# Kernel tuning notes

Hardware: AMD Instinct MI355X
Metric: run time of the kernel (lower is better)

Reference implementation:

```python
import jax, jax.numpy as jnp
import numpy as np

SEQ_LEN = 8192
HIDDEN = 4096

def setup_inputs() -> dict:
    key = jax.random.key(0)
    k1, k2 = jax.random.split(key)
    hidden = jax.random.normal(k1, (HIDDEN,), dtype=jnp.float32)
    encoder_outputs = jax.random.normal(k2, (SEQ_LEN, 1, HIDDEN), dtype=jnp.float32)
    return {"hidden": hidden, "encoder_outputs": encoder_outputs}

def reference(hidden, encoder_outputs):
    # encoder_outputs: [S, 1, H] -> [S, H]
    enc = encoder_outputs.squeeze(1)
    # energies[i] = dot(hidden, enc[i])  (one batched GEMV instead of a per-step loop)
    energies = enc @ hidden  # [S]
    attn = jax.nn.softmax(energies, axis=0)  # [S]
    # output = enc^T @ attn  (torch.mm(enc.T, attn.unsqueeze(1)).squeeze(1))
    output = enc.T @ attn  # [H]
    return output, attn[:, None]
```

## Files before the change

### kernel.cpp

```cpp
#include <hip/hip_runtime.h>
#include <math.h>

#define S_LEN 8192
#define HDIM  4096
#define H4    (HDIM / 4)
#define P1_BLOCK 512
#define P1_WAVES 8
#define RB 4
#define FB_ATTN 8

__device__ __forceinline__ float wave_reduce_sum(float x) {
#pragma unroll
  for (int o = 32; o > 0; o >>= 1) x += __shfl_xor(x, o, 64);
  return x;
}
__device__ __forceinline__ float wave_reduce_max(float x) {
#pragma unroll
  for (int o = 32; o > 0; o >>= 1) x = fmaxf(x, __shfl_xor(x, o, 64));
  return x;
}
__device__ __forceinline__ float dot4(float4 a, float4 b) {
  return a.x * b.x + a.y * b.y + a.z * b.z + a.w * b.w;
}
__device__ __forceinline__ float upd(float a, float sc, const float* w,
                                     float x0, float x1, float x2, float x3) {
  float r = a * sc;
  r = fmaf(w[0], x0, r);
  r = fmaf(w[1], x1, r);
  r = fmaf(w[2], x2, r);
  r = fmaf(w[3], x3, r);
  return r;
}

__global__ __launch_bounds__(P1_BLOCK) void pass1_k(
    const float* __restrict__ enc, const float* __restrict__ hidden,
    float* __restrict__ energies, float* __restrict__ mb, float* __restrict__ lb,
    float* __restrict__ opart, int rpb) {
  const int t = threadIdx.x;
  const int b = blockIdx.x;
  const int row0 = b * rpb;
  const int row1 = min(S_LEN, row0 + rpb);

  const float4* hv = (const float4*)hidden;
  const float4 h0 = hv[t];
  const float4 h1 = hv[t + P1_BLOCK];

  float4 a0 = {0.f, 0.f, 0.f, 0.f};
  float4 a1 = {0.f, 0.f, 0.f, 0.f};
  float m = -INFINITY, l = 0.f;

  __shared__ float red[RB * P1_WAVES];
  const int wid = t >> 6;
  const bool lane0 = (t & 63) == 0;
  const float4* encv = (const float4*)enc;

  for (int r0 = row0; r0 < row1; r0 += RB) {
    const int nr = min(RB, row1 - r0);
    float4 v[RB][2];
    float d[RB];
#pragma unroll
    for (int r = 0; r < RB; ++r) {
      if (r < nr) {
        const float4* rp = encv + (size_t)(r0 + r) * H4;
        v[r][0] = rp[t];
        v[r][1] = rp[t + P1_BLOCK];
      } else {
        v[r][0] = make_float4(0.f, 0.f, 0.f, 0.f);
        v[r][1] = make_float4(0.f, 0.f, 0.f, 0.f);
      }
    }
#pragma unroll
    for (int r = 0; r < RB; ++r)
      d[r] = dot4(v[r][0], h0) + dot4(v[r][1], h1);
#pragma unroll
    for (int o = 32; o > 0; o >>= 1) {
#pragma unroll
      for (int r = 0; r < RB; ++r) d[r] += __shfl_xor(d[r], o, 64);
    }
    if (lane0) {
#pragma unroll
      for (int r = 0; r < RB; ++r) red[r * P1_WAVES + wid] = d[r];
    }
    __syncthreads();
    float e[RB];
#pragma unroll
    for (int r = 0; r < RB; ++r) {
      const float4 q0 = *(const float4*)&red[r * P1_WAVES];
      const float4 q1 = *(const float4*)&red[r * P1_WAVES + 4];
      e[r] = (q0.x + q0.y + q0.z + q0.w) + (q1.x + q1.y + q1.z + q1.w);
    }
    __syncthreads();
    if (t == 0) {
      for (int r = 0; r < nr; ++r) energies[r0 + r] = e[r];
    }
    float mn = m;
#pragma unroll
    for (int r = 0; r < RB; ++r)
      if (r < nr) mn = fmaxf(mn, e[r]);
    const float sc = __expf(m - mn);
    float w[RB];
#pragma unroll
    for (int r = 0; r < RB; ++r) w[r] = (r < nr) ? __expf(e[r] - mn) : 0.f;
    l = l * sc + w[0] + w[1] + w[2] + w[3];
    a0.x = upd(a0.x, sc, w, v[0][0].x, v[1][0].x, v[2][0].x, v[3][0].x);
    a0.y = upd(a0.y, sc, w, v[0][0].y, v[1][0].y, v[2][0].y, v[3][0].y);
    a0.z = upd(a0.z, sc, w, v[0][0].z, v[1][0].z, v[2][0].z, v[3][0].z);
    a0.w = upd(a0.w, sc, w, v[0][0].w, v[1][0].w, v[2][0].w, v[3][0].w);
    a1.x = upd(a1.x, sc, w, v[0][1].x, v[1][1].x, v[2][1].x, v[3][1].x);
    a1.y = upd(a1.y, sc, w, v[0][1].y, v[1][1].y, v[2][1].y, v[3][1].y);
    a1.z = upd(a1.z, sc, w, v[0][1].z, v[1][1].z, v[2][1].z, v[3][1].z);
    a1.w = upd(a1.w, sc, w, v[0][1].w, v[1][1].w, v[2][1].w, v[3][1].w);
    m = mn;
  }

  float4* op = (float4*)(opart + (size_t)b * HDIM);
  op[t] = a0;
  op[t + P1_BLOCK] = a1;
  if (t == 0) { mb[b] = m; lb[b] = l; }
}

__global__ __launch_bounds__(256) void finalize_k(
    const float* __restrict__ opart, const float* __restrict__ mb,
    const float* __restrict__ lb, const float* __restrict__ energies,
    float* __restrict__ out, int Gu, int Bout, int gpb) {
  const int t = threadIdx.x;
  const int wid = t >> 6;
  const bool lane0 = (t & 63) == 0;
  __shared__ float smax[4], ssum[4];

  float mv = -INFINITY;
  for (int g = t; g < Gu; g += 256) mv = fmaxf(mv, mb[g]);
  mv = wave_reduce_max(mv);
  if (lane0) smax[wid] = mv;
  __syncthreads();
  const float gm = fmaxf(fmaxf(smax[0], smax[1]), fmaxf(smax[2], smax[3]));

  float lv = 0.f;
  for (int g = t; g < Gu; g += 256) lv += lb[g] * __expf(mb[g] - gm);
  lv = wave_reduce_sum(lv);
  if (lane0) ssum[wid] = lv;
  __syncthreads();
  const float invL = 1.f / (ssum[0] + ssum[1] + ssum[2] + ssum[3]);

  if ((int)blockIdx.x < Bout) {
    const int g0 = blockIdx.x * gpb;
    const int g1 = min(Gu, g0 + gpb);
    float4 acc[4] = {{0,0,0,0},{0,0,0,0},{0,0,0,0},{0,0,0,0}};
    for (int g = g0; g < g1; ++g) {
      const float w = __expf(mb[g] - gm) * invL;
      const float4* op = (const float4*)(opart + (size_t)g * HDIM);
#pragma unroll
      for (int k = 0; k < 4; ++k) {
        const float4 v = op[t + k * 256];
        acc[k].x = fmaf(w, v.x, acc[k].x);
        acc[k].y = fmaf(w, v.y, acc[k].y);
        acc[k].z = fmaf(w, v.z, acc[k].z);
        acc[k].w = fmaf(w, v.w, acc[k].w);
      }
    }
#pragma unroll
    for (int k = 0; k < 4; ++k) {
      const int h = (t + k * 256) * 4;
      atomicAdd(&out[h + 0], acc[k].x);
      atomicAdd(&out[h + 1], acc[k].y);
      atomicAdd(&out[h + 2], acc[k].z);
      atomicAdd(&out[h + 3], acc[k].w);
    }
  } else {
    const int i4 = ((int)blockIdx.x - Bout) * 256 + t;
    const float4 e = ((const float4*)energies)[i4];
    float4 a;
    a.x = __expf(e.x - gm) * invL;
    a.y = __expf(e.y - gm) * invL;
    a.z = __expf(e.z - gm) * invL;
    a.w = __expf(e.w - gm) * invL;
    ((float4*)(out + HDIM))[i4] = a;
  }
}

extern "C" void kernel_launch(void* const* d_in, const int* in_sizes, int n_in,
                              void* d_out, int out_size, void* d_ws, size_t ws_size,
                              hipStream_t stream) {
  const float* hidden = (const float*)d_in[0];
  const float* enc    = (const float*)d_in[1];
  float* out = (float*)d_out;
  float* wsf = (float*)d_ws;

  float* energies = wsf;
  float* mb       = wsf + 8192;
  float* lb       = wsf + 9216;
  float* opart    = wsf + 10240;

  const size_t avail_f = ws_size / 4;
  int Gmax = (avail_f > 10240) ? (int)((avail_f - 10240) / HDIM) : 1;
  int G = Gmax < 512 ? Gmax : 512;
  if (G < 1) G = 1;
  const int rpb = (S_LEN + G - 1) / G;
  const int Gu  = (S_LEN + rpb - 1) / rpb;

  hipMemsetAsync(d_out, 0, HDIM * sizeof(float), stream);
  pass1_k<<<Gu, P1_BLOCK, 0, stream>>>(enc, hidden, energies, mb, lb, opart, rpb);

  int Bout = Gu < 128 ? Gu : 128;
  const int gpb = (Gu + Bout - 1) / Bout;
  Bout = (Gu + gpb - 1) / gpb;
  finalize_k<<<Bout + FB_ATTN, 256, 0, stream>>>(opart, mb, lb, energies, out, Gu, Bout, gpb);
}
```

Baseline: 210.9 us.

## Widen row batch to 8 and replace atomic finalize with column-split reduction

The first pass now processes 8 encoder rows per iteration instead of 4, which doubles the loads in flight per thread and halves the number of block syncs per row. The finalize kernel is restructured so each of 32 blocks owns a column slice and reduces over all partials through shared memory, then writes the output directly. This removes the atomicAdds and the memset launch. The cost is higher register pressure in pass1 and fewer blocks doing the output reduction.

```diff
diff --git a/kernel.cpp b/kernel.cpp
--- a/kernel.cpp
+++ b/kernel.cpp
@@ -6,7 +6,8 @@
 #define H4    (HDIM / 4)
 #define P1_BLOCK 512
 #define P1_WAVES 8
-#define RB 4
+#define RB 8
+#define SUMB 32
 #define FB_ATTN 8
 
 __device__ __forceinline__ float wave_reduce_sum(float x) {
@@ -18,18 +19,6 @@
 #pragma unroll
   for (int o = 32; o > 0; o >>= 1) x = fmaxf(x, __shfl_xor(x, o, 64));
   return x;
-}
-__device__ __forceinline__ float dot4(float4 a, float4 b) {
-  return a.x * b.x + a.y * b.y + a.z * b.z + a.w * b.w;
-}
-__device__ __forceinline__ float upd(float a, float sc, const float* w,
-                                     float x0, float x1, float x2, float x3) {
-  float r = a * sc;
-  r = fmaf(w[0], x0, r);
-  r = fmaf(w[1], x1, r);
-  r = fmaf(w[2], x2, r);
-  r = fmaf(w[3], x3, r);
-  return r;
 }
 
 __global__ __launch_bounds__(P1_BLOCK) void pass1_k(
@@ -42,11 +31,15 @@
   const int row1 = min(S_LEN, row0 + rpb);
 
   const float4* hv = (const float4*)hidden;
-  const float4 h0 = hv[t];
-  const float4 h1 = hv[t + P1_BLOCK];
-
-  float4 a0 = {0.f, 0.f, 0.f, 0.f};
-  float4 a1 = {0.f, 0.f, 0.f, 0.f};
+  float hh[8];
+  {
+    const float4 h0 = hv[t];
+    const float4 h1 = hv[t + P1_BLOCK];
+    hh[0] = h0.x; hh[1] = h0.y; hh[2] = h0.z; hh[3] = h0.w;
+    hh[4] = h1.x; hh[5] = h1.y; hh[6] = h1.z; hh[7] = h1.w;
+  }
+
+  float aa[8] = {0.f, 0.f, 0.f, 0.f, 0.f, 0.f, 0.f, 0.f};
   float m = -INFINITY, l = 0.f;
 
   __shared__ float red[RB * P1_WAVES];
@@ -56,22 +49,27 @@
 
   for (int r0 = row0; r0 < row1; r0 += RB) {
     const int nr = min(RB, row1 - r0);
-    float4 v[RB][2];
+    float vv[RB][8];
     float d[RB];
 #pragma unroll
     for (int r = 0; r < RB; ++r) {
+      float4 x0 = make_float4(0.f, 0.f, 0.f, 0.f);
+      float4 x1 = make_float4(0.f, 0.f, 0.f, 0.f);
       if (r < nr) {
         const float4* rp = encv + (size_t)(r0 + r) * H4;
-        v[r][0] = rp[t];
-        v[r][1] = rp[t + P1_BLOCK];
-      } else {
-        v[r][0] = make_float4(0.f, 0.f, 0.f, 0.f);
-        v[r][1] = make_float4(0.f, 0.f, 0.f, 0.f);
+        x0 = rp[t];
+        x1 = rp[t + P1_BLOCK];
       }
-    }
-#pragma unroll
-    for (int r = 0; r < RB; ++r)
-      d[r] = dot4(v[r][0], h0) + dot4(v[r][1], h1);
+      vv[r][0] = x0.x; vv[r][1] = x0.y; vv[r][2] = x0.z; vv[r][3] = x0.w;
+      vv[r][4] = x1.x; vv[r][5] = x1.y; vv[r][6] = x1.z; vv[r][7] = x1.w;
+    }
+#pragma unroll
+    for (int r = 0; r < RB; ++r) {
+      float s = 0.f;
+#pragma unroll
+      for (int k = 0; k < 8; ++k) s = fmaf(vv[r][k], hh[k], s);
+      d[r] = s;
+    }
 #pragma unroll
     for (int o = 32; o > 0; o >>= 1) {
 #pragma unroll
@@ -99,30 +97,33 @@
       if (r < nr) mn = fmaxf(mn, e[r]);
     const float sc = __expf(m - mn);
     float w[RB];
-#pragma unroll
-    for (int r = 0; r < RB; ++r) w[r] = (r < nr) ? __expf(e[r] - mn) : 0.f;
-    l = l * sc + w[0] + w[1] + w[2] + w[3];
-    a0.x = upd(a0.x, sc, w, v[0][0].x, v[1][0].x, v[2][0].x, v[3][0].x);
-    a0.y = upd(a0.y, sc, w, v[0][0].y, v[1][0].y, v[2][0].y, v[3][0].y);
-    a0.z = upd(a0.z, sc, w, v[0][0].z, v[1][0].z, v[2][0].z, v[3][0].z);
-    a0.w = upd(a0.w, sc, w, v[0][0].w, v[1][0].w, v[2][0].w, v[3][0].w);
-    a1.x = upd(a1.x, sc, w, v[0][1].x, v[1][1].x, v[2][1].x, v[3][1].x);
-    a1.y = upd(a1.y, sc, w, v[0][1].y, v[1][1].y, v[2][1].y, v[3][1].y);
-    a1.z = upd(a1.z, sc, w, v[0][1].z, v[1][1].z, v[2][1].z, v[3][1].z);
-    a1.w = upd(a1.w, sc, w, v[0][1].w, v[1][1].w, v[2][1].w, v[3][1].w);
+    float lsum = 0.f;
+#pragma unroll
+    for (int r = 0; r < RB; ++r) {
+      w[r] = (r < nr) ? __expf(e[r] - mn) : 0.f;
+      lsum += w[r];
+    }
+    l = l * sc + lsum;
+#pragma unroll
+    for (int k = 0; k < 8; ++k) {
+      float a = aa[k] * sc;
+#pragma unroll
+      for (int r = 0; r < RB; ++r) a = fmaf(w[r], vv[r][k], a);
+      aa[k] = a;
+    }
     m = mn;
   }
 
   float4* op = (float4*)(opart + (size_t)b * HDIM);
-  op[t] = a0;
-  op[t + P1_BLOCK] = a1;
+  op[t]            = make_float4(aa[0], aa[1], aa[2], aa[3]);
+  op[t + P1_BLOCK] = make_float4(aa[4], aa[5], aa[6], aa[7]);
   if (t == 0) { mb[b] = m; lb[b] = l; }
 }
 
 __global__ __launch_bounds__(256) void finalize_k(
     const float* __restrict__ opart, const float* __restrict__ mb,
     const float* __restrict__ lb, const float* __restrict__ energies,
-    float* __restrict__ out, int Gu, int Bout, int gpb) {
+    float* __restrict__ out, int Gu) {
   const int t = threadIdx.x;
   const int wid = t >> 6;
   const bool lane0 = (t & 63) == 0;
@@ -142,32 +143,32 @@
   __syncthreads();
   const float invL = 1.f / (ssum[0] + ssum[1] + ssum[2] + ssum[3]);
 
-  if ((int)blockIdx.x < Bout) {
-    const int g0 = blockIdx.x * gpb;
-    const int g1 = min(Gu, g0 + gpb);
-    float4 acc[4] = {{0,0,0,0},{0,0,0,0},{0,0,0,0},{0,0,0,0}};
-    for (int g = g0; g < g1; ++g) {
+  if ((int)blockIdx.x < SUMB) {
+    const int c  = blockIdx.x * 32 + (t & 31);
+    const int g0 = t >> 5;
+    float4 acc = {0.f, 0.f, 0.f, 0.f};
+    for (int g = g0; g < Gu; g += 8) {
       const float w = __expf(mb[g] - gm) * invL;
-      const float4* op = (const float4*)(opart + (size_t)g * HDIM);
-#pragma unroll
-      for (int k = 0; k < 4; ++k) {
-        const float4 v = op[t + k * 256];
-        acc[k].x = fmaf(w, v.x, acc[k].x);
-        acc[k].y = fmaf(w, v.y, acc[k].y);
-        acc[k].z = fmaf(w, v.z, acc[k].z);
-        acc[k].w = fmaf(w, v.w, acc[k].w);
+      const float4 v = ((const float4*)opart)[(size_t)g * H4 + c];
+      acc.x = fmaf(w, v.x, acc.x);
+      acc.y = fmaf(w, v.y, acc.y);
+      acc.z = fmaf(w, v.z, acc.z);
+      acc.w = fmaf(w, v.w, acc.w);
+    }
+    __shared__ float4 sred[256];
+    sred[t] = acc;
+    __syncthreads();
+    if (t < 32) {
+      float4 s = sred[t];
+#pragma unroll
+      for (int q = 1; q < 8; ++q) {
+        const float4 v = sred[q * 32 + t];
+        s.x += v.x; s.y += v.y; s.z += v.z; s.w += v.w;
       }
-    }
-#pragma unroll
-    for (int k = 0; k < 4; ++k) {
-      const int h = (t + k * 256) * 4;
-      atomicAdd(&out[h + 0], acc[k].x);
-      atomicAdd(&out[h + 1], acc[k].y);
-      atomicAdd(&out[h + 2], acc[k].z);
-      atomicAdd(&out[h + 3], acc[k].w);
+      ((float4*)out)[blockIdx.x * 32 + t] = s;
     }
   } else {
-    const int i4 = ((int)blockIdx.x - Bout) * 256 + t;
+    const int i4 = ((int)blockIdx.x - SUMB) * 256 + t;
     const float4 e = ((const float4*)energies)[i4];
     float4 a;
     a.x = __expf(e.x - gm) * invL;
@@ -198,11 +199,6 @@
   const int rpb = (S_LEN + G - 1) / G;
   const int Gu  = (S_LEN + rpb - 1) / rpb;
 
-  hipMemsetAsync(d_out, 0, HDIM * sizeof(float), stream);
   pass1_k<<<Gu, P1_BLOCK, 0, stream>>>(enc, hidden, energies, mb, lb, opart, rpb);
-
-  int Bout = Gu < 128 ? Gu : 128;
-  const int gpb = (Gu + Bout - 1) / Bout;
-  Bout = (Gu + gpb - 1) / gpb;
-  finalize_k<<<Bout + FB_ATTN, 256, 0, stream>>>(opart, mb, lb, energies, out, Gu, Bout, gpb);
-}
+  finalize_k<<<SUMB + FB_ATTN, 256, 0, stream>>>(opart, mb, lb, energies, out, Gu);
+}
```

Result: no change. 211.9 us (+0.5%).
